# Kernel optimization log

Hardware: AMD Instinct MI355X
Metric: run time of the kernel (lower is better)

Reference implementation:

```python
import jax, jax.numpy as jnp
import numpy as np

W_MAE, W_GRAD, W_TV, W_BG, W_MSE = 1.0, 0.1, 0.002, 0.15, 1.0
EPS = 1e-8


def setup_inputs() -> dict:
    key = jax.random.key(0)
    k1, k2, k3 = jax.random.split(key, 3)
    B, C, D, H, W = 2, 3, 128, 128, 128
    pred = jax.random.normal(k1, (B, C, D, H, W), dtype=jnp.float32)
    target = jax.random.normal(k2, (B, C, D, H, W), dtype=jnp.float32)
    # binary foreground mask, broadcast over channels
    mask = (jax.random.uniform(k3, (B, 1, D, H, W)) > 0.5).astype(jnp.float32)
    return {"pred": pred, "target": target, "mask": mask}


def _grad3(x):
    dx = x[:, :, 1:, :, :] - x[:, :, :-1, :, :]
    dy = x[:, :, :, 1:, :] - x[:, :, :, :-1, :]
    dz = x[:, :, :, :, 1:] - x[:, :, :, :, :-1]
    return dx, dy, dz


def reference(pred, target, mask):
    C = pred.shape[1]

    def masked_mean(x, m):
        return (x * m).sum() / (m.sum() * C + EPS)

    pred_in = pred * mask
    tgt_in = target * mask
    diff = pred_in - tgt_in

    l_mae = masked_mean(jnp.abs(diff), mask)

    px, py, pz = _grad3(pred_in)
    tx, ty, tz = _grad3(tgt_in)
    mx = jnp.minimum(mask[:, :, 1:, :, :], mask[:, :, :-1, :, :])
    my = jnp.minimum(mask[:, :, :, 1:, :], mask[:, :, :, :-1, :])
    mz = jnp.minimum(mask[:, :, :, :, 1:], mask[:, :, :, :, :-1])

    l_grad = (masked_mean(jnp.abs(px - tx), mx)
              + masked_mean(jnp.abs(py - ty), my)
              + masked_mean(jnp.abs(pz - tz), mz))
    l_tv = (masked_mean(jnp.abs(px), mx)
            + masked_mean(jnp.abs(py), my)
            + masked_mean(jnp.abs(pz), mz))

    inv = 1.0 - mask
    l_bg = (jnp.abs(pred) * inv).sum() / (inv.sum() * C + EPS)

    l_mse = masked_mean(diff ** 2, mask)

    return (W_MAE * l_mae + W_GRAD * l_grad + W_TV * l_tv
            + W_BG * l_bg + W_MSE * l_mse)
```

## Files before the change

kernel.cpp:

```cpp
#include <hip/hip_runtime.h>

#define NACC 13
#define NPAD 16
#define NBLOCKS 4096
#define NROWS 16384
#define NMID 64

__device__ __forceinline__ float4 ld4(const float* p) {
    return *reinterpret_cast<const float4*>(p);
}

__global__ __launch_bounds__(256) void loss_main(
    const float* __restrict__ pred, const float* __restrict__ target,
    const float* __restrict__ mask, float* __restrict__ partials)
{
    float acc[NACC];
#pragma unroll
    for (int k = 0; k < NACC; ++k) acc[k] = 0.f;

    const int g  = blockIdx.x * 256 + threadIdx.x;
    const int w4 = g & 31;
    const int h  = (g >> 5) & 127;
    const int d  = (g >> 12) & 127;
    const int b  = g >> 19;
    const int w  = w4 << 2;
    const int mb  = b * 2097152 + d * 16384 + h * 128 + w;
    const int pb0 = b * 6291456 + d * 16384 + h * 128 + w;

    const float wv = (w4 < 31) ? 1.f : 0.f;
    const float hv = (h < 127) ? 1.f : 0.f;
    const float dv = (d < 127) ? 1.f : 0.f;
    const int oh = (h < 127) ? 128   : 0;
    const int od = (d < 127) ? 16384 : 0;

    const float4 m0  = ld4(mask + mb);
    const float4 mh  = ld4(mask + mb + oh);
    const float4 md  = ld4(mask + mb + od);
    const float  m4w = __shfl_down(m0.x, 1, 64);

    const float mz0 = fminf(m0.x, m0.y), mz1 = fminf(m0.y, m0.z),
                mz2 = fminf(m0.z, m0.w), mz3 = fminf(m0.w, m4w) * wv;
    const float my0 = fminf(m0.x, mh.x) * hv, my1 = fminf(m0.y, mh.y) * hv,
                my2 = fminf(m0.z, mh.z) * hv, my3 = fminf(m0.w, mh.w) * hv;
    const float mx0 = fminf(m0.x, md.x) * dv, mx1 = fminf(m0.y, md.y) * dv,
                mx2 = fminf(m0.z, md.z) * dv, mx3 = fminf(m0.w, md.w) * dv;

    acc[0] = m0.x + m0.y + m0.z + m0.w;
    acc[1] = mx0 + mx1 + mx2 + mx3;
    acc[2] = my0 + my1 + my2 + my3;
    acc[3] = mz0 + mz1 + mz2 + mz3;

#pragma unroll
    for (int c = 0; c < 3; ++c) {
        const int pb = pb0 + c * 2097152;
        const float4 p0 = ld4(pred + pb);
        const float4 t0 = ld4(target + pb);
        const float4 ph = ld4(pred + pb + oh);
        const float4 th = ld4(target + pb + oh);
        const float4 pd = ld4(pred + pb + od);
        const float4 td = ld4(target + pb + od);
        const float  p4 = __shfl_down(p0.x, 1, 64);
        const float  t4 = __shfl_down(t0.x, 1, 64);

        const float e0x = p0.x - t0.x, e0y = p0.y - t0.y,
                    e0z = p0.z - t0.z, e0w = p0.w - t0.w;
        const float e4  = p4 - t4;

        acc[4] += fabsf(e0x)*m0.x + fabsf(e0y)*m0.y
                + fabsf(e0z)*m0.z + fabsf(e0w)*m0.w;
        acc[5] += e0x*e0x*m0.x + e0y*e0y*m0.y
                + e0z*e0z*m0.z + e0w*e0w*m0.w;
        acc[6] += fabsf(p0.x)*(1.f-m0.x) + fabsf(p0.y)*(1.f-m0.y)
                + fabsf(p0.z)*(1.f-m0.z) + fabsf(p0.w)*(1.f-m0.w);

        acc[9]  += fabsf(e0y-e0x)*mz0 + fabsf(e0z-e0y)*mz1
                 + fabsf(e0w-e0z)*mz2 + fabsf(e4 -e0w)*mz3;
        acc[12] += fabsf(p0.y-p0.x)*mz0 + fabsf(p0.z-p0.y)*mz1
                 + fabsf(p0.w-p0.z)*mz2 + fabsf(p4  -p0.w)*mz3;

        acc[8]  += fabsf((ph.x-th.x)-e0x)*my0 + fabsf((ph.y-th.y)-e0y)*my1
                 + fabsf((ph.z-th.z)-e0z)*my2 + fabsf((ph.w-th.w)-e0w)*my3;
        acc[11] += fabsf(ph.x-p0.x)*my0 + fabsf(ph.y-p0.y)*my1
                 + fabsf(ph.z-p0.z)*my2 + fabsf(ph.w-p0.w)*my3;

        acc[7]  += fabsf((pd.x-td.x)-e0x)*mx0 + fabsf((pd.y-td.y)-e0y)*mx1
                 + fabsf((pd.z-td.z)-e0z)*mx2 + fabsf((pd.w-td.w)-e0w)*mx3;
        acc[10] += fabsf(pd.x-p0.x)*mx0 + fabsf(pd.y-p0.y)*mx1
                 + fabsf(pd.z-p0.z)*mx2 + fabsf(pd.w-p0.w)*mx3;
    }

    const int lane = threadIdx.x & 63;
    const int wave = threadIdx.x >> 6;
    float mine = 0.f;
#pragma unroll
    for (int k = 0; k < NACC; ++k) {
        float v = acc[k];
        for (int o = 32; o > 0; o >>= 1) v += __shfl_down(v, o, 64);
        const float tot = __shfl(v, 0, 64);
        if (lane == k) mine = tot;
    }
    if (lane < NPAD)
        partials[(blockIdx.x * 4 + wave) * NPAD + lane] = mine;
}

__global__ __launch_bounds__(256) void loss_mid(
    const float* __restrict__ partials, float* __restrict__ mid)
{
    const int r = blockIdx.x * 256 + threadIdx.x;
    const float* row = partials + r * NPAD;
    const float4 r0 = ld4(row);     const float4 r1 = ld4(row + 4);
    const float4 r2 = ld4(row + 8); const float4 r3 = ld4(row + 12);
    float acc[NPAD] = {r0.x, r0.y, r0.z, r0.w, r1.x, r1.y, r1.z, r1.w,
                       r2.x, r2.y, r2.z, r2.w, r3.x, r3.y, r3.z, r3.w};

    const int lane = threadIdx.x & 63;
    const int wave = threadIdx.x >> 6;
    __shared__ float red[4][NPAD];
#pragma unroll
    for (int k = 0; k < NPAD; ++k) {
        float v = acc[k];
        for (int o = 32; o > 0; o >>= 1) v += __shfl_down(v, o, 64);
        if (lane == 0) red[wave][k] = v;
    }
    __syncthreads();
    if (threadIdx.x < NPAD) {
        const int k = threadIdx.x;
        mid[blockIdx.x * NPAD + k] =
            red[0][k] + red[1][k] + red[2][k] + red[3][k];
    }
}

__global__ __launch_bounds__(64) void loss_final(
    const float* __restrict__ mid, float* __restrict__ out)
{
    const int lane = threadIdx.x;
    float acc[NPAD];
    {
        const float* row = mid + lane * NPAD;
        const float4 r0 = ld4(row);     const float4 r1 = ld4(row + 4);
        const float4 r2 = ld4(row + 8); const float4 r3 = ld4(row + 12);
        acc[0] = r0.x;  acc[1] = r0.y;  acc[2] = r0.z;  acc[3] = r0.w;
        acc[4] = r1.x;  acc[5] = r1.y;  acc[6] = r1.z;  acc[7] = r1.w;
        acc[8] = r2.x;  acc[9] = r2.y;  acc[10] = r2.z; acc[11] = r2.w;
        acc[12] = r3.x; acc[13] = r3.y; acc[14] = r3.z; acc[15] = r3.w;
    }
#pragma unroll
    for (int k = 0; k < NACC; ++k) {
        for (int o = 32; o > 0; o >>= 1) acc[k] += __shfl_down(acc[k], o, 64);
    }
    if (lane == 0) {
        const float EPS = 1e-8f;
        const float M = acc[0], Mx = acc[1], My = acc[2], Mz = acc[3];
        float loss = (acc[4] + acc[5]) / (3.f * M + EPS);
        loss += 0.1f   * (acc[7] / (3.f*Mx + EPS) + acc[8] / (3.f*My + EPS)
                        + acc[9] / (3.f*Mz + EPS));
        loss += 0.002f * (acc[10] / (3.f*Mx + EPS) + acc[11] / (3.f*My + EPS)
                        + acc[12] / (3.f*Mz + EPS));
        const float inv = 4194304.f - M;
        loss += 0.15f * acc[6] / (3.f * inv + EPS);
        out[0] = loss;
    }
}

extern "C" void kernel_launch(void* const* d_in, const int* in_sizes, int n_in,
                              void* d_out, int out_size, void* d_ws, size_t ws_size,
                              hipStream_t stream) {
    const float* pred   = (const float*)d_in[0];
    const float* target = (const float*)d_in[1];
    const float* mask   = (const float*)d_in[2];
    float* out      = (float*)d_out;
    float* partials = (float*)d_ws;
    float* mid      = partials + NROWS * NPAD;

    loss_main<<<NBLOCKS, 256, 0, stream>>>(pred, target, mask, partials);
    loss_mid<<<NMID, 256, 0, stream>>>(partials, mid);
    loss_final<<<1, 64, 0, stream>>>(mid, out);
}
```

Baseline: 143.8 us.

## Stage 2x4x128 tile with halos into LDS via direct global-to-LDS loads

Each block now covers a 2-deep, 4-row slab plus its +1 halo in d and h for mask, pred and target. The slab is copied into shared memory with global_load_lds async copies, and all neighbour reads are served from LDS instead of separate global float4 loads. This cuts redundant global and L2 traffic for the h/d neighbours, which the old kernel loaded three times per element. In exchange it uses about 50KB of LDS per block, which may limit occupancy, and it adds a sync barrier before compute.

```diff
diff --git a/kernel.cpp b/kernel.cpp
--- a/kernel.cpp
+++ b/kernel.cpp
@@ -10,33 +10,70 @@
     return *reinterpret_cast<const float4*>(p);
 }
 
+__device__ __forceinline__ void gload16(const float* g, float4* l) {
+    __builtin_amdgcn_global_load_lds(
+        (const __attribute__((address_space(1))) void*)g,
+        (__attribute__((address_space(3))) void*)l, 16, 0, 0);
+}
+
 __global__ __launch_bounds__(256) void loss_main(
     const float* __restrict__ pred, const float* __restrict__ target,
     const float* __restrict__ mask, float* __restrict__ partials)
 {
-    float acc[NACC];
-#pragma unroll
-    for (int k = 0; k < NACC; ++k) acc[k] = 0.f;
-
-    const int g  = blockIdx.x * 256 + threadIdx.x;
-    const int w4 = g & 31;
-    const int h  = (g >> 5) & 127;
-    const int d  = (g >> 12) & 127;
-    const int b  = g >> 19;
-    const int w  = w4 << 2;
-    const int mb  = b * 2097152 + d * 16384 + h * 128 + w;
-    const int pb0 = b * 6291456 + d * 16384 + h * 128 + w;
-
+    __shared__ float4 smem[3136];
+
+    const int tid  = threadIdx.x;
+    const int lane = tid & 63;
+    const int wav  = tid >> 6;
+
+    const int bid  = blockIdx.x;
+    const int h0   = (bid & 31) << 2;
+    const int d0   = ((bid >> 5) & 63) << 1;
+    const int b    = bid >> 11;
+
+#pragma unroll
+    for (int j = 0; j < 13; ++j) {
+        const int o = wav + (j << 2);
+        if (o >= 49) break;
+        const int a  = o / 7;
+        const int oi = o - a * 7;
+        const int q  = (oi << 6) + lane;
+        const int w4 = q & 31;
+        int dl, hl;
+        if (oi < 4)      { dl = q >> 7;        hl = (q >> 5) & 3; }
+        else if (oi < 6) { dl = 2;             hl = (q >> 5) & 3; }
+        else             { dl = (q >> 5) & 1;  hl = 4; }
+        int d = d0 + dl; d = (d > 127) ? 127 : d;
+        int h = h0 + hl; h = (h > 127) ? 127 : h;
+        const int sp = d * 16384 + h * 128 + (w4 << 2);
+        const float* gp;
+        if (a == 0)     gp = mask   + b * 2097152 + sp;
+        else if (a < 4) gp = pred   + (3 * b + a - 1) * 2097152 + sp;
+        else            gp = target + (3 * b + a - 4) * 2097152 + sp;
+        gload16(gp, &smem[(o << 6) + lane]);
+    }
+    __syncthreads();
+
+    const int w4 = tid & 31;
+    const int hl = (tid >> 5) & 3;
+    const int dl = tid >> 7;
+    const int d  = d0 + dl, h = h0 + hl;
     const float wv = (w4 < 31) ? 1.f : 0.f;
     const float hv = (h < 127) ? 1.f : 0.f;
     const float dv = (d < 127) ? 1.f : 0.f;
-    const int oh = (h < 127) ? 128   : 0;
-    const int od = (d < 127) ? 16384 : 0;
-
-    const float4 m0  = ld4(mask + mb);
-    const float4 mh  = ld4(mask + mb + oh);
-    const float4 md  = ld4(mask + mb + od);
-    const float  m4w = __shfl_down(m0.x, 1, 64);
+
+    const int qs = tid;
+    const int qh = (hl < 3)  ? (tid + 32)  : (384 + (dl << 5) + w4);
+    const int qd = (dl == 0) ? (tid + 128) : (256 + (hl << 5) + w4);
+
+    float acc[NACC];
+#pragma unroll
+    for (int k = 0; k < NACC; ++k) acc[k] = 0.f;
+
+    const float4 m0 = smem[qs];
+    const float4 mh = smem[qh];
+    const float4 md = smem[qd];
+    const float m4w = __shfl_down(m0.x, 1, 64);
 
     const float mz0 = fminf(m0.x, m0.y), mz1 = fminf(m0.y, m0.z),
                 mz2 = fminf(m0.z, m0.w), mz3 = fminf(m0.w, m4w) * wv;
@@ -52,13 +89,12 @@
 
 #pragma unroll
     for (int c = 0; c < 3; ++c) {
-        const int pb = pb0 + c * 2097152;
-        const float4 p0 = ld4(pred + pb);
-        const float4 t0 = ld4(target + pb);
-        const float4 ph = ld4(pred + pb + oh);
-        const float4 th = ld4(target + pb + oh);
-        const float4 pd = ld4(pred + pb + od);
-        const float4 td = ld4(target + pb + od);
+        const float4 p0 = smem[(1 + c) * 448 + qs];
+        const float4 t0 = smem[(4 + c) * 448 + qs];
+        const float4 ph = smem[(1 + c) * 448 + qh];
+        const float4 th = smem[(4 + c) * 448 + qh];
+        const float4 pd = smem[(1 + c) * 448 + qd];
+        const float4 td = smem[(4 + c) * 448 + qd];
         const float  p4 = __shfl_down(p0.x, 1, 64);
         const float  t4 = __shfl_down(t0.x, 1, 64);
 
@@ -89,8 +125,6 @@
                  + fabsf(pd.z-p0.z)*mx2 + fabsf(pd.w-p0.w)*mx3;
     }
 
-    const int lane = threadIdx.x & 63;
-    const int wave = threadIdx.x >> 6;
     float mine = 0.f;
 #pragma unroll
     for (int k = 0; k < NACC; ++k) {
@@ -100,7 +134,7 @@
         if (lane == k) mine = tot;
     }
     if (lane < NPAD)
-        partials[(blockIdx.x * 4 + wave) * NPAD + lane] = mine;
+        partials[(bid * 4 + wav) * NPAD + lane] = mine;
 }
 
 __global__ __launch_bounds__(256) void loss_mid(
```

Measured after the change: 144.0 us. Within noise of the previous version (+0.1%).
